# Performance work log

Hardware: AMD Instinct MI355X
Metric: run time of the kernel (lower is better)

Reference implementation:

```python
import jax, jax.numpy as jnp
import numpy as np

B = 256          # batch of molecules
N_ATOM = 1024    # atoms per molecule
N_EDGE = 8192    # directed edges per molecule (avg degree 8)
NEG_SLOPE = 0.01 # torch LeakyReLU default


def setup_inputs() -> dict:
    key = jax.random.key(0)
    ks = jax.random.split(key, 8)
    x = jax.random.normal(ks[0], (B, 3 * N_ATOM), dtype=jnp.float32)
    edge_index = jax.random.randint(ks[1], (2, N_EDGE), 0, N_ATOM, dtype=jnp.int64)
    # GCNConv weights (Glorot-ish small scale) and biases
    W1 = jax.random.normal(ks[2], (3, 64), dtype=jnp.float32) * 0.3
    b1 = jnp.zeros((64,), jnp.float32)
    W2 = jax.random.normal(ks[3], (64, 64), dtype=jnp.float32) * 0.1
    b2 = jnp.zeros((64,), jnp.float32)
    # project MLP: Linear(64,128) + LeakyReLU
    Wp = jax.random.normal(ks[4], (64, 128), dtype=jnp.float32) * 0.1
    bp = jnp.zeros((128,), jnp.float32)
    return {"x": x, "edge_index": edge_index, "W1": W1, "b1": b1,
            "W2": W2, "b2": b2, "Wp": Wp, "bp": bp}


def _leaky_relu(v):
    return jnp.where(v >= 0, v, NEG_SLOPE * v)


def reference(x, edge_index, W1, b1, W2, b2, Wp, bp):
    # x: [B, 3*n_atom] -> node features [B, n_atom, 3]
    bsz, n_feat = x.shape
    n = n_feat // 3
    h = x.reshape(bsz, n, 3)

    src = edge_index[0]  # message sources
    dst = edge_index[1]  # aggregation targets

    # GCN normalization with self-loops: deg[i] = 1 + in-degree(i)
    ones_e = jnp.ones((src.shape[0],), x.dtype)
    deg = jax.ops.segment_sum(ones_e, dst, num_segments=n) + 1.0
    dinv = jax.lax.rsqrt(deg)                # deg^{-1/2}, deg >= 1
    norm_e = dinv[src] * dinv[dst]           # [E]
    norm_self = dinv * dinv                  # self-loop weight per node

    def gcn(h, W, b):
        hw = h @ W                                        # [B, n, d_out]
        msg = hw[:, src, :] * norm_e[None, :, None]       # [B, E, d_out]
        agg = jax.vmap(lambda m: jax.ops.segment_sum(m, dst, num_segments=n))(msg)
        return agg + norm_self[None, :, None] * hw + b

    h = _leaky_relu(gcn(h, W1, b1))
    h = _leaky_relu(gcn(h, W2, b2))

    # global_mean_pool: every graph has exactly n atoms -> mean over atom axis
    g = h.mean(axis=1)                                    # [B, 64]

    # project MLP: Linear + LeakyReLU
    return _leaky_relu(g @ Wp + bp)                       # [B, 128]
```

## Files before the change

### kernel.cpp

```cpp
#include <hip/hip_runtime.h>

#define N_ATOMS 1024
#define N_EDGES 8192
#define EPAD    (N_EDGES + N_ATOMS)
#define NBATCH  256
#define NEG     0.01f

typedef unsigned int u32;
typedef __attribute__((ext_vector_type(2))) float f32x2;
typedef __attribute__((ext_vector_type(4))) float f32x4;
typedef __attribute__((ext_vector_type(8))) _Float16 f16x8;

__device__ __forceinline__ u32 pkrtz(float lo, float hi) {
    u32 r;
    asm("v_cvt_pkrtz_f16_f32 %0, %1, %2" : "=v"(r) : "v"(lo), "v"(hi));
    return r;
}
#define FMIX_LO(a, w, u) \
    asm("v_fma_mix_f32 %0, %1, %2, %0 op_sel_hi:[0,1,0]" : "+v"(a) : "v"(w), "v"(u))
#define FMIX_HI(a, w, u) \
    asm("v_fma_mix_f32 %0, %1, %2, %0 op_sel:[0,1,0] op_sel_hi:[0,1,0]" : "+v"(a) : "v"(w), "v"(u))

#define ROWPTR_OFF 0
#define COLW_OFF   4352
#define SELFW_OFF  (4352 + 73728)
#define PERM_OFF   (SELFW_OFF + 4096)
#define W2T_OFF    (PERM_OFF + 4096)

#define TSTR_B 144
#define SM_TILE_BYTES (N_ATOMS * TSTR_B)
#define SM_CT_OFF SM_TILE_BYTES
#define SM_TOTAL (SM_TILE_BYTES + 16384)

__global__ __launch_bounds__(1024) void build_csr(
    const int* __restrict__ ei,
    int*  __restrict__ rowptr,
    int2* __restrict__ colw,
    float* __restrict__ selfw_g,
    int*  __restrict__ perm_g,
    u32*  __restrict__ w2t,
    const float* __restrict__ W2)
{
    __shared__ int   sdeg[N_ATOMS];
    __shared__ int   sstart[N_ATOMS];
    __shared__ float sdinv[N_ATOMS];
    __shared__ int   wtot[16];
    __shared__ int   hist[128];
    const int t = threadIdx.x;
    const int lane = t & 63;
    const int w = t >> 6;
    const int* srcA = ei;
    const int* dstA = ei + N_EDGES;

    sdeg[t] = 0;
    if (t < 128) hist[t] = 0;
    for (int e = t; e < EPAD; e += 1024) colw[e] = make_int2(0, 0);
    __syncthreads();
    for (int e = t; e < N_EDGES; e += 1024) atomicAdd(&sdeg[dstA[e]], 1);
    __syncthreads();

    const int deg  = sdeg[t];
    const int pdeg = (deg + 1) & ~1;
    int v = pdeg;
    #pragma unroll
    for (int d = 1; d < 64; d <<= 1) {
        int u = __shfl_up(v, d, 64);
        if (lane >= d) v += u;
    }
    if (lane == 63) wtot[w] = v;
    __syncthreads();
    if (t == 0) {
        int run = 0;
        #pragma unroll
        for (int i = 0; i < 16; ++i) { int c = wtot[i]; wtot[i] = run; run += c; }
    }
    __syncthreads();
    const int start = v - pdeg + wtot[w];
    sstart[t] = start;
    const float dv = rsqrtf((float)deg + 1.0f);
    sdinv[t] = dv;
    rowptr[t] = start;
    if (t == N_ATOMS - 1) rowptr[N_ATOMS] = start + pdeg;
    selfw_g[t] = dv * dv;

    #pragma unroll
    for (int i = 0; i < 2; ++i) {
        const int idx = t + i * 1024;
        const int c = idx >> 5, kk = idx & 31;
        w2t[c * 32 + kk] = pkrtz(W2[(2 * kk) * 64 + c], W2[(2 * kk + 1) * 64 + c]);
    }

    const int dcl = deg < 127 ? deg : 127;
    atomicAdd(&hist[dcl], 1);
    sdeg[t] = 0;
    __syncthreads();
    if (t == 0) {
        int run = 0;
        for (int i = 0; i < 128; ++i) { int c = hist[i]; hist[i] = run; run += c; }
    }
    __syncthreads();
    const int pos = atomicAdd(&hist[dcl], 1);
    perm_g[pos] = t;
    __syncthreads();

    for (int e = t; e < N_EDGES; e += 1024) {
        const int d = dstA[e];
        const int s = srcA[e];
        const int slot = atomicAdd(&sdeg[d], 1);
        const float wgt = sdinv[s] * sdinv[d];
        colw[sstart[d] + slot] = make_int2(s, __float_as_int(wgt));
    }
}

__global__ __launch_bounds__(1024, 4) void gnn_main(
    const float* __restrict__ x,
    const int*  __restrict__ rowptr,
    const int2* __restrict__ colw,
    const float* __restrict__ selfw_g,
    const int*  __restrict__ perm_g,
    const float* __restrict__ W1, const float* __restrict__ b1,
    const u32*  __restrict__ w2t, const float* __restrict__ b2,
    const float* __restrict__ Wp, const float* __restrict__ bp,
    float* __restrict__ out)
{
    extern __shared__ char smem[];
    float4* ctile4 = (float4*)(smem + SM_CT_OFF);
    float*  paux   = (float*)ctile4;
    float*  wpool  = paux;
    float*  gvec   = paux + 1024;
    float*  proj   = paux + 1088;

    const int t = threadIdx.x;
    const int b = blockIdx.x;
    const float* xb = x + (size_t)b * (3 * N_ATOMS);

    const int atom = perm_g[t];
    const int s0 = rowptr[atom], s1 = rowptr[atom + 1];
    const float sw = selfw_g[atom];

    {
        float4 c;
        c.x = xb[3 * t]; c.y = xb[3 * t + 1]; c.z = xb[3 * t + 2]; c.w = 0.0f;
        ctile4[t] = c;
    }
    __syncthreads();

    u32 pw[32];
    {
        const float4 cs = ctile4[atom];
        float A0 = sw * cs.x, A1 = sw * cs.y, A2 = sw * cs.z;
        int4 cur = make_int4(0, 0, 0, 0);
        if (s0 < s1) cur = *(const int4*)(colw + s0);
        for (int j = s0; j < s1; j += 2) {
            const int jn = (j + 2 < s1) ? (j + 2) : s0;
            const int4 nxt = *(const int4*)(colw + jn);
            const float4 c0 = ctile4[cur.x];
            const float4 c1 = ctile4[cur.z];
            const float w0 = __int_as_float(cur.y), w1 = __int_as_float(cur.w);
            A0 += w0 * c0.x + w1 * c1.x;
            A1 += w0 * c0.y + w1 * c1.y;
            A2 += w0 * c0.z + w1 * c1.z;
            cur = nxt;
        }
        #pragma unroll
        for (int p = 0; p < 32; ++p) {
            f32x2 vv = *(const f32x2*)(b1 + 2 * p);
            vv = __builtin_elementwise_fma((f32x2){A0, A0}, *(const f32x2*)(W1 + 2 * p), vv);
            vv = __builtin_elementwise_fma((f32x2){A1, A1}, *(const f32x2*)(W1 + 64 + 2 * p), vv);
            vv = __builtin_elementwise_fma((f32x2){A2, A2}, *(const f32x2*)(W1 + 128 + 2 * p), vv);
            vv.x = fmaxf(vv.x, NEG * vv.x);
            vv.y = fmaxf(vv.y, NEG * vv.y);
            pw[p] = pkrtz(vv.x, vv.y);
        }
        uint4* trow = (uint4*)(smem + (size_t)atom * TSTR_B);
        #pragma unroll
        for (int q = 0; q < 8; ++q)
            trow[q] = make_uint4(pw[4 * q], pw[4 * q + 1], pw[4 * q + 2], pw[4 * q + 3]);
    }
    __syncthreads();

    float acc[64];
    {
        #pragma unroll
        for (int f = 0; f < 64; ++f) acc[f] = 0.0f;
        #pragma unroll
        for (int p = 0; p < 32; ++p) {
            FMIX_LO(acc[2 * p],     sw, pw[p]);
            FMIX_HI(acc[2 * p + 1], sw, pw[p]);
        }
        int4 cur = make_int4(0, 0, 0, 0);
        if (s0 < s1) cur = *(const int4*)(colw + s0);
        for (int j = s0; j < s1; j += 2) {
            const int jn = (j + 2 < s1) ? (j + 2) : s0;
            const int4 nxt = *(const int4*)(colw + jn);
            const uint4* rA = (const uint4*)(smem + (size_t)cur.x * TSTR_B);
            const uint4* rB = (const uint4*)(smem + (size_t)cur.z * TSTR_B);
            const float wA = __int_as_float(cur.y);
            const float wB = __int_as_float(cur.w);
            #pragma unroll
            for (int m = 0; m < 8; ++m) {
                const uint4 qA = rA[m];
                FMIX_LO(acc[8*m+0], wA, qA.x); FMIX_HI(acc[8*m+1], wA, qA.x);
                FMIX_LO(acc[8*m+2], wA, qA.y); FMIX_HI(acc[8*m+3], wA, qA.y);
                FMIX_LO(acc[8*m+4], wA, qA.z); FMIX_HI(acc[8*m+5], wA, qA.z);
                FMIX_LO(acc[8*m+6], wA, qA.w); FMIX_HI(acc[8*m+7], wA, qA.w);
            }
            #pragma unroll
            for (int m = 0; m < 8; ++m) {
                const uint4 qB = rB[m];
                FMIX_LO(acc[8*m+0], wB, qB.x); FMIX_HI(acc[8*m+1], wB, qB.x);
                FMIX_LO(acc[8*m+2], wB, qB.y); FMIX_HI(acc[8*m+3], wB, qB.y);
                FMIX_LO(acc[8*m+4], wB, qB.z); FMIX_HI(acc[8*m+5], wB, qB.z);
                FMIX_LO(acc[8*m+6], wB, qB.w); FMIX_HI(acc[8*m+7], wB, qB.w);
            }
            cur = nxt;
        }
    }
    __syncthreads();

    {
        u32 pb[32];
        #pragma unroll
        for (int p = 0; p < 32; ++p) pb[p] = pkrtz(acc[2 * p], acc[2 * p + 1]);
        uint4* trow = (uint4*)(smem + (size_t)atom * TSTR_B);
        #pragma unroll
        for (int q = 0; q < 8; ++q)
            trow[q] = make_uint4(pb[4 * q], pb[4 * q + 1], pb[4 * q + 2], pb[4 * q + 3]);
    }

    {
        const int l15 = t & 15;
        const int lq  = (t & 63) >> 4;
        const int w   = t >> 6;

        f16x8 wf[2][4];
        #pragma unroll
        for (int kt = 0; kt < 2; ++kt)
            #pragma unroll
            for (int ct = 0; ct < 4; ++ct)
                wf[kt][ct] = *(const f16x8*)(w2t + (ct * 16 + l15) * 32 + kt * 16 + lq * 4);
        float bias[4];
        #pragma unroll
        for (int ct = 0; ct < 4; ++ct) bias[ct] = b2[ct * 16 + l15];

        float pool[4] = {0.f, 0.f, 0.f, 0.f};
        #pragma unroll
        for (int rt = 0; rt < 4; ++rt) {
            const int arow = __shfl(atom, rt * 16 + l15, 64);
            const char* ab = smem + (size_t)arow * TSTR_B + lq * 16;
            const f16x8 a0 = *(const f16x8*)(ab);
            const f16x8 a1 = *(const f16x8*)(ab + 64);
            #pragma unroll
            for (int ct = 0; ct < 4; ++ct) {
                f32x4 cf = {0.f, 0.f, 0.f, 0.f};
                cf = __builtin_amdgcn_mfma_f32_16x16x32_f16(a0, wf[0][ct], cf, 0, 0, 0);
                cf = __builtin_amdgcn_mfma_f32_16x16x32_f16(a1, wf[1][ct], cf, 0, 0, 0);
                float s = 0.0f;
                #pragma unroll
                for (int r = 0; r < 4; ++r) {
                    const float vv = cf[r] + bias[ct];
                    s += fmaxf(vv, NEG * vv);
                }
                pool[ct] += s;
            }
        }
        #pragma unroll
        for (int ct = 0; ct < 4; ++ct) {
            pool[ct] += __shfl_xor(pool[ct], 16, 64);
            pool[ct] += __shfl_xor(pool[ct], 32, 64);
        }
        if ((t & 63) < 16) {
            #pragma unroll
            for (int ct = 0; ct < 4; ++ct)
                wpool[w * 64 + ct * 16 + l15] = pool[ct];
        }
    }
    __syncthreads();

    if (t < 64) {
        float s = 0.0f;
        #pragma unroll
        for (int w = 0; w < 16; ++w) s += wpool[w * 64 + t];
        gvec[t] = s * (1.0f / 1024.0f);
    }
    __syncthreads();
    if (t < 512) {
        const int col = t & 127, pc = t >> 7;
        float s = 0.0f;
        #pragma unroll
        for (int f = 0; f < 16; ++f)
            s += gvec[pc * 16 + f] * Wp[(pc * 16 + f) * 128 + col];
        proj[pc * 128 + col] = s;
    }
    __syncthreads();
    if (t < 128) {
        float s = bp[t] + proj[t] + proj[128 + t] + proj[256 + t] + proj[384 + t];
        s = fmaxf(s, NEG * s);
        out[(size_t)b * 128 + t] = s;
    }
}

extern "C" void kernel_launch(void* const* d_in, const int* in_sizes, int n_in,
                              void* d_out, int out_size, void* d_ws, size_t ws_size,
                              hipStream_t stream) {
    const float* x  = (const float*)d_in[0];
    const int*   ei = (const int*)  d_in[1];
    const float* W1 = (const float*)d_in[2];
    const float* b1 = (const float*)d_in[3];
    const float* W2 = (const float*)d_in[4];
    const float* b2 = (const float*)d_in[5];
    const float* Wp = (const float*)d_in[6];
    const float* bp = (const float*)d_in[7];
    float* out = (float*)d_out;

    char* ws = (char*)d_ws;
    int*   rowptr = (int*)  (ws + ROWPTR_OFF);
    int2*  colw   = (int2*) (ws + COLW_OFF);
    float* selfw  = (float*)(ws + SELFW_OFF);
    int*   perm   = (int*)  (ws + PERM_OFF);
    u32*   w2t    = (u32*)  (ws + W2T_OFF);

    build_csr<<<1, 1024, 0, stream>>>(ei, rowptr, colw, selfw, perm, w2t, W2);

    (void)hipFuncSetAttribute((const void*)gnn_main,
                              hipFuncAttributeMaxDynamicSharedMemorySize, SM_TOTAL);
    gnn_main<<<NBATCH, 1024, SM_TOTAL, stream>>>(
        x, rowptr, colw, selfw, perm, W1, b1, w2t, b2, Wp, bp, out);
}
```

Measured before the change: 39.28 us.

## Split second-layer aggregation across 8 lanes per atom by feature slice

The layer-2 neighbor aggregation is restructured so each atom is handled by 8 threads, each accumulating a 16-byte (8-feature) slice over 8 atoms, instead of one thread accumulating all 64 features for one atom. This cuts per-thread accumulator registers from 64 to 8 per atom, which should help occupancy. It also spreads LDS row reads across lanes and balances degree variation differently. The atom-to-row mapping for the MFMA stage now comes from a shared-memory table rather than a shuffle, at the cost of an extra store and more colw/rowptr global reads, since each edge list is now read by 8 lanes.

```diff
diff --git a/kernel.cpp b/kernel.cpp
--- a/kernel.cpp
+++ b/kernel.cpp
@@ -129,14 +129,11 @@
     float*  wpool  = paux;
     float*  gvec   = paux + 1024;
     float*  proj   = paux + 1088;
+    int*    satom  = (int*)(paux + 1600);
 
     const int t = threadIdx.x;
     const int b = blockIdx.x;
     const float* xb = x + (size_t)b * (3 * N_ATOMS);
-
-    const int atom = perm_g[t];
-    const int s0 = rowptr[atom], s1 = rowptr[atom + 1];
-    const float sw = selfw_g[atom];
 
     {
         float4 c;
@@ -145,8 +142,10 @@
     }
     __syncthreads();
 
-    u32 pw[32];
     {
+        const int atom = perm_g[t];
+        const int s0 = rowptr[atom], s1 = rowptr[atom + 1];
+        const float sw = selfw_g[atom];
         const float4 cs = ctile4[atom];
         float A0 = sw * cs.x, A1 = sw * cs.y, A2 = sw * cs.z;
         int4 cur = make_int4(0, 0, 0, 0);
@@ -162,6 +161,7 @@
             A2 += w0 * c0.z + w1 * c1.z;
             cur = nxt;
         }
+        u32 pw[32];
         #pragma unroll
         for (int p = 0; p < 32; ++p) {
             f32x2 vv = *(const f32x2*)(b1 + 2 * p);
@@ -179,59 +179,72 @@
     }
     __syncthreads();
 
-    float acc[64];
-    {
-        #pragma unroll
-        for (int f = 0; f < 64; ++f) acc[f] = 0.0f;
-        #pragma unroll
-        for (int p = 0; p < 32; ++p) {
-            FMIX_LO(acc[2 * p],     sw, pw[p]);
-            FMIX_HI(acc[2 * p + 1], sw, pw[p]);
-        }
-        int4 cur = make_int4(0, 0, 0, 0);
-        if (s0 < s1) cur = *(const int4*)(colw + s0);
-        for (int j = s0; j < s1; j += 2) {
-            const int jn = (j + 2 < s1) ? (j + 2) : s0;
-            const int4 nxt = *(const int4*)(colw + jn);
-            const uint4* rA = (const uint4*)(smem + (size_t)cur.x * TSTR_B);
-            const uint4* rB = (const uint4*)(smem + (size_t)cur.z * TSTR_B);
-            const float wA = __int_as_float(cur.y);
-            const float wB = __int_as_float(cur.w);
-            #pragma unroll
-            for (int m = 0; m < 8; ++m) {
-                const uint4 qA = rA[m];
-                FMIX_LO(acc[8*m+0], wA, qA.x); FMIX_HI(acc[8*m+1], wA, qA.x);
-                FMIX_LO(acc[8*m+2], wA, qA.y); FMIX_HI(acc[8*m+3], wA, qA.y);
-                FMIX_LO(acc[8*m+4], wA, qA.z); FMIX_HI(acc[8*m+5], wA, qA.z);
-                FMIX_LO(acc[8*m+6], wA, qA.w); FMIX_HI(acc[8*m+7], wA, qA.w);
-            }
-            #pragma unroll
-            for (int m = 0; m < 8; ++m) {
-                const uint4 qB = rB[m];
-                FMIX_LO(acc[8*m+0], wB, qB.x); FMIX_HI(acc[8*m+1], wB, qB.x);
-                FMIX_LO(acc[8*m+2], wB, qB.y); FMIX_HI(acc[8*m+3], wB, qB.y);
-                FMIX_LO(acc[8*m+4], wB, qB.z); FMIX_HI(acc[8*m+5], wB, qB.z);
-                FMIX_LO(acc[8*m+6], wB, qB.w); FMIX_HI(acc[8*m+7], wB, qB.w);
-            }
-            cur = nxt;
-        }
-    }
-    __syncthreads();
-
-    {
-        u32 pb[32];
-        #pragma unroll
-        for (int p = 0; p < 32; ++p) pb[p] = pkrtz(acc[2 * p], acc[2 * p + 1]);
-        uint4* trow = (uint4*)(smem + (size_t)atom * TSTR_B);
-        #pragma unroll
-        for (int q = 0; q < 8; ++q)
-            trow[q] = make_uint4(pb[4 * q], pb[4 * q + 1], pb[4 * q + 2], pb[4 * q + 3]);
-    }
+    const int w   = t >> 6;
+    const int g   = (t & 63) >> 3;
+    const int m   = t & 7;
+    const int mo  = m * 16;
+
+    int atoms[8];
+    #pragma unroll
+    for (int k = 0; k < 8; ++k) atoms[k] = perm_g[k * 128 + w * 8 + g];
+    int s0a[8], s1a[8];
+    #pragma unroll
+    for (int k = 0; k < 8; ++k) {
+        s0a[k] = rowptr[atoms[k]];
+        s1a[k] = rowptr[atoms[k] + 1];
+    }
+
+    u32 pr[8][4];
+    #pragma unroll
+    for (int k = 0; k < 8; ++k) {
+        const int atom = atoms[k];
+        float acc[8];
+        #pragma unroll
+        for (int f = 0; f < 8; ++f) acc[f] = 0.0f;
+        {
+            const float swk = selfw_g[atom];
+            const uint4 sv = *(const uint4*)(smem + (size_t)atom * TSTR_B + mo);
+            FMIX_LO(acc[0], swk, sv.x); FMIX_HI(acc[1], swk, sv.x);
+            FMIX_LO(acc[2], swk, sv.y); FMIX_HI(acc[3], swk, sv.y);
+            FMIX_LO(acc[4], swk, sv.z); FMIX_HI(acc[5], swk, sv.z);
+            FMIX_LO(acc[6], swk, sv.w); FMIX_HI(acc[7], swk, sv.w);
+        }
+        for (int j = s0a[k]; j < s1a[k]; j += 2) {
+            const int4 cw = *(const int4*)(colw + j);
+            const uint4 qA = *(const uint4*)(smem + (size_t)cw.x * TSTR_B + mo);
+            const uint4 qB = *(const uint4*)(smem + (size_t)cw.z * TSTR_B + mo);
+            const float wA = __int_as_float(cw.y);
+            const float wB = __int_as_float(cw.w);
+            FMIX_LO(acc[0], wA, qA.x); FMIX_HI(acc[1], wA, qA.x);
+            FMIX_LO(acc[2], wA, qA.y); FMIX_HI(acc[3], wA, qA.y);
+            FMIX_LO(acc[4], wA, qA.z); FMIX_HI(acc[5], wA, qA.z);
+            FMIX_LO(acc[6], wA, qA.w); FMIX_HI(acc[7], wA, qA.w);
+            FMIX_LO(acc[0], wB, qB.x); FMIX_HI(acc[1], wB, qB.x);
+            FMIX_LO(acc[2], wB, qB.y); FMIX_HI(acc[3], wB, qB.y);
+            FMIX_LO(acc[4], wB, qB.z); FMIX_HI(acc[5], wB, qB.z);
+            FMIX_LO(acc[6], wB, qB.w); FMIX_HI(acc[7], wB, qB.w);
+        }
+        pr[k][0] = pkrtz(acc[0], acc[1]);
+        pr[k][1] = pkrtz(acc[2], acc[3]);
+        pr[k][2] = pkrtz(acc[4], acc[5]);
+        pr[k][3] = pkrtz(acc[6], acc[7]);
+    }
+    __syncthreads();
+
+    #pragma unroll
+    for (int k = 0; k < 8; ++k) {
+        *(uint4*)(smem + (size_t)atoms[k] * TSTR_B + mo) =
+            make_uint4(pr[k][0], pr[k][1], pr[k][2], pr[k][3]);
+    }
+    if (m == 0) {
+        #pragma unroll
+        for (int k = 0; k < 8; ++k) satom[w * 64 + k * 8 + g] = atoms[k];
+    }
+    __syncthreads();
 
     {
         const int l15 = t & 15;
         const int lq  = (t & 63) >> 4;
-        const int w   = t >> 6;
 
         f16x8 wf[2][4];
         #pragma unroll
@@ -246,7 +259,7 @@
         float pool[4] = {0.f, 0.f, 0.f, 0.f};
         #pragma unroll
         for (int rt = 0; rt < 4; ++rt) {
-            const int arow = __shfl(atom, rt * 16 + l15, 64);
+            const int arow = satom[w * 64 + rt * 16 + l15];
             const char* ab = smem + (size_t)arow * TSTR_B + lq * 16;
             const f16x8 a0 = *(const f16x8*)(ab);
             const f16x8 a1 = *(const f16x8*)(ab + 64);
@@ -280,7 +293,7 @@
     if (t < 64) {
         float s = 0.0f;
         #pragma unroll
-        for (int w = 0; w < 16; ++w) s += wpool[w * 64 + t];
+        for (int ww = 0; ww < 16; ++ww) s += wpool[ww * 64 + t];
         gvec[t] = s * (1.0f / 1024.0f);
     }
     __syncthreads();
```

Result: slower. 41.93 us (+6.7%).

## Split fused GNN kernel into h1, gather and projection kernels via global fp16 buffer

Applied to the files above, without the earlier changes.

The single per-molecule kernel, which needed about 160 KB of LDS and ran one block per molecule, is split into three kernels. k_h1 writes layer-1 fp16 features to a 32 MB global workspace. k_gather runs 8 blocks per molecule, with the block index swizzled by XCD, and reads neighbour rows from global/L2. It applies the W2 MFMA and accumulates the pooled sums with atomics. k_proj then does the final projection. The aim is higher occupancy and parallelism than the LDS-bound single block gave, at the cost of extra global memory traffic, more kernel launches and float atomics that make results order-dependent.

```diff
diff --git a/kernel.cpp b/kernel.cpp
--- a/kernel.cpp
+++ b/kernel.cpp
@@ -26,11 +26,8 @@
 #define SELFW_OFF  (4352 + 73728)
 #define PERM_OFF   (SELFW_OFF + 4096)
 #define W2T_OFF    (PERM_OFF + 4096)
-
-#define TSTR_B 144
-#define SM_TILE_BYTES (N_ATOMS * TSTR_B)
-#define SM_CT_OFF SM_TILE_BYTES
-#define SM_TOTAL (SM_TILE_BYTES + 16384)
+#define H1_OFF     131072
+#define POOL_OFF   (H1_OFF + 33554432)
 
 __global__ __launch_bounds__(1024) void build_csr(
     const int* __restrict__ ei,
@@ -39,7 +36,8 @@
     float* __restrict__ selfw_g,
     int*  __restrict__ perm_g,
     u32*  __restrict__ w2t,
-    const float* __restrict__ W2)
+    const float* __restrict__ W2,
+    float* __restrict__ pool)
 {
     __shared__ int   sdeg[N_ATOMS];
     __shared__ int   sstart[N_ATOMS];
@@ -54,7 +52,8 @@
 
     sdeg[t] = 0;
     if (t < 128) hist[t] = 0;
-    for (int e = t; e < EPAD; e += 1024) colw[e] = make_int2(0, 0);
+    #pragma unroll
+    for (int i = t; i < NBATCH * 64; i += 1024) pool[i] = 0.0f;
     __syncthreads();
     for (int e = t; e < N_EDGES; e += 1024) atomicAdd(&sdeg[dstA[e]], 1);
     __syncthreads();
@@ -82,6 +81,7 @@
     rowptr[t] = start;
     if (t == N_ATOMS - 1) rowptr[N_ATOMS] = start + pdeg;
     selfw_g[t] = dv * dv;
+    if (deg & 1) colw[start + deg] = make_int2(0, 0);
 
     #pragma unroll
     for (int i = 0; i < 2; ++i) {
@@ -112,31 +112,19 @@
     }
 }
 
-__global__ __launch_bounds__(1024, 4) void gnn_main(
+__global__ __launch_bounds__(1024) void k_h1(
     const float* __restrict__ x,
     const int*  __restrict__ rowptr,
     const int2* __restrict__ colw,
     const float* __restrict__ selfw_g,
     const int*  __restrict__ perm_g,
     const float* __restrict__ W1, const float* __restrict__ b1,
-    const u32*  __restrict__ w2t, const float* __restrict__ b2,
-    const float* __restrict__ Wp, const float* __restrict__ bp,
-    float* __restrict__ out)
+    char* __restrict__ h1b)
 {
-    extern __shared__ char smem[];
-    float4* ctile4 = (float4*)(smem + SM_CT_OFF);
-    float*  paux   = (float*)ctile4;
-    float*  wpool  = paux;
-    float*  gvec   = paux + 1024;
-    float*  proj   = paux + 1088;
-
+    __shared__ float4 ctile4[N_ATOMS];
     const int t = threadIdx.x;
     const int b = blockIdx.x;
     const float* xb = x + (size_t)b * (3 * N_ATOMS);
-
-    const int atom = perm_g[t];
-    const int s0 = rowptr[atom], s1 = rowptr[atom + 1];
-    const float sw = selfw_g[atom];
 
     {
         float4 c;
@@ -145,93 +133,123 @@
     }
     __syncthreads();
 
+    const int atom = perm_g[t];
+    const int s0 = rowptr[atom], s1 = rowptr[atom + 1];
+    const float sw = selfw_g[atom];
+    const float4 cs = ctile4[atom];
+    float A0 = sw * cs.x, A1 = sw * cs.y, A2 = sw * cs.z;
+    int4 cur = make_int4(0, 0, 0, 0);
+    if (s0 < s1) cur = *(const int4*)(colw + s0);
+    for (int j = s0; j < s1; j += 2) {
+        const int jn = (j + 2 < s1) ? (j + 2) : s0;
+        const int4 nxt = *(const int4*)(colw + jn);
+        const float4 c0 = ctile4[cur.x];
+        const float4 c1 = ctile4[cur.z];
+        const float w0 = __int_as_float(cur.y), w1 = __int_as_float(cur.w);
+        A0 += w0 * c0.x + w1 * c1.x;
+        A1 += w0 * c0.y + w1 * c1.y;
+        A2 += w0 * c0.z + w1 * c1.z;
+        cur = nxt;
+    }
     u32 pw[32];
+    #pragma unroll
+    for (int p = 0; p < 32; ++p) {
+        f32x2 vv = *(const f32x2*)(b1 + 2 * p);
+        vv = __builtin_elementwise_fma((f32x2){A0, A0}, *(const f32x2*)(W1 + 2 * p), vv);
+        vv = __builtin_elementwise_fma((f32x2){A1, A1}, *(const f32x2*)(W1 + 64 + 2 * p), vv);
+        vv = __builtin_elementwise_fma((f32x2){A2, A2}, *(const f32x2*)(W1 + 128 + 2 * p), vv);
+        vv.x = fmaxf(vv.x, NEG * vv.x);
+        vv.y = fmaxf(vv.y, NEG * vv.y);
+        pw[p] = pkrtz(vv.x, vv.y);
+    }
+    uint4* row = (uint4*)(h1b + ((size_t)b << 17) + (size_t)atom * 128);
+    #pragma unroll
+    for (int q = 0; q < 8; ++q)
+        row[q] = make_uint4(pw[4 * q], pw[4 * q + 1], pw[4 * q + 2], pw[4 * q + 3]);
+}
+
+__global__ __launch_bounds__(256, 5) void k_gather(
+    const char* __restrict__ h1b,
+    const int*  __restrict__ rowptr,
+    const int2* __restrict__ colw,
+    const float* __restrict__ selfw_g,
+    const int*  __restrict__ perm_g,
+    const u32*  __restrict__ w2t, const float* __restrict__ b2,
+    float* __restrict__ pool)
+{
+    __shared__ char stg[128 * 144];
+    const int bid = blockIdx.x;
+    const int xcd = bid & 7, inner = bid >> 3;
+    const int seg = inner & 7, m32 = inner >> 3;
+    const int b = xcd + (m32 << 3);
+    const char* h1 = h1b + ((size_t)b << 17);
+
+    const int t = threadIdx.x;
+    const int slot = t >> 1, half = t & 1;
+    const int ho = half * 64;
+
+    const int atom = perm_g[slot * 8 + seg];
+    const int r0 = rowptr[atom];
+    const int np = (rowptr[atom + 1] - r0) >> 1;
+    const float swk = selfw_g[atom];
+
+    float acc[32];
+    #pragma unroll
+    for (int f = 0; f < 32; ++f) acc[f] = 0.0f;
+
     {
-        const float4 cs = ctile4[atom];
-        float A0 = sw * cs.x, A1 = sw * cs.y, A2 = sw * cs.z;
-        int4 cur = make_int4(0, 0, 0, 0);
-        if (s0 < s1) cur = *(const int4*)(colw + s0);
-        for (int j = s0; j < s1; j += 2) {
-            const int jn = (j + 2 < s1) ? (j + 2) : s0;
-            const int4 nxt = *(const int4*)(colw + jn);
-            const float4 c0 = ctile4[cur.x];
-            const float4 c1 = ctile4[cur.z];
-            const float w0 = __int_as_float(cur.y), w1 = __int_as_float(cur.w);
-            A0 += w0 * c0.x + w1 * c1.x;
-            A1 += w0 * c0.y + w1 * c1.y;
-            A2 += w0 * c0.z + w1 * c1.z;
-            cur = nxt;
-        }
-        #pragma unroll
-        for (int p = 0; p < 32; ++p) {
-            f32x2 vv = *(const f32x2*)(b1 + 2 * p);
-            vv = __builtin_elementwise_fma((f32x2){A0, A0}, *(const f32x2*)(W1 + 2 * p), vv);
-            vv = __builtin_elementwise_fma((f32x2){A1, A1}, *(const f32x2*)(W1 + 64 + 2 * p), vv);
-            vv = __builtin_elementwise_fma((f32x2){A2, A2}, *(const f32x2*)(W1 + 128 + 2 * p), vv);
-            vv.x = fmaxf(vv.x, NEG * vv.x);
-            vv.y = fmaxf(vv.y, NEG * vv.y);
-            pw[p] = pkrtz(vv.x, vv.y);
-        }
-        uint4* trow = (uint4*)(smem + (size_t)atom * TSTR_B);
-        #pragma unroll
-        for (int q = 0; q < 8; ++q)
-            trow[q] = make_uint4(pw[4 * q], pw[4 * q + 1], pw[4 * q + 2], pw[4 * q + 3]);
-    }
-    __syncthreads();
-
-    float acc[64];
+        const uint4* own = (const uint4*)(h1 + (size_t)atom * 128 + ho);
+        #pragma unroll
+        for (int q = 0; q < 4; ++q) {
+            const uint4 sv = own[q];
+            FMIX_LO(acc[q*8+0], swk, sv.x); FMIX_HI(acc[q*8+1], swk, sv.x);
+            FMIX_LO(acc[q*8+2], swk, sv.y); FMIX_HI(acc[q*8+3], swk, sv.y);
+            FMIX_LO(acc[q*8+4], swk, sv.z); FMIX_HI(acc[q*8+5], swk, sv.z);
+            FMIX_LO(acc[q*8+6], swk, sv.w); FMIX_HI(acc[q*8+7], swk, sv.w);
+        }
+    }
+    int4 cur = make_int4(0, 0, 0, 0);
+    if (np > 0) cur = *(const int4*)(colw + r0);
+    for (int j = 0; j < np; ++j) {
+        const int4 nxt = (j + 1 < np) ? *(const int4*)(colw + r0 + 2 * (j + 1)) : cur;
+        const uint4* rA = (const uint4*)(h1 + (size_t)cur.x * 128 + ho);
+        const uint4* rB = (const uint4*)(h1 + (size_t)cur.z * 128 + ho);
+        const float wA = __int_as_float(cur.y);
+        const float wB = __int_as_float(cur.w);
+        #pragma unroll
+        for (int q = 0; q < 4; ++q) {
+            const uint4 qa = rA[q];
+            FMIX_LO(acc[q*8+0], wA, qa.x); FMIX_HI(acc[q*8+1], wA, qa.x);
+            FMIX_LO(acc[q*8+2], wA, qa.y); FMIX_HI(acc[q*8+3], wA, qa.y);
+            FMIX_LO(acc[q*8+4], wA, qa.z); FMIX_HI(acc[q*8+5], wA, qa.z);
+            FMIX_LO(acc[q*8+6], wA, qa.w); FMIX_HI(acc[q*8+7], wA, qa.w);
+        }
+        #pragma unroll
+        for (int q = 0; q < 4; ++q) {
+            const uint4 qb = rB[q];
+            FMIX_LO(acc[q*8+0], wB, qb.x); FMIX_HI(acc[q*8+1], wB, qb.x);
+            FMIX_LO(acc[q*8+2], wB, qb.y); FMIX_HI(acc[q*8+3], wB, qb.y);
+            FMIX_LO(acc[q*8+4], wB, qb.z); FMIX_HI(acc[q*8+5], wB, qb.z);
+            FMIX_LO(acc[q*8+6], wB, qb.w); FMIX_HI(acc[q*8+7], wB, qb.w);
+        }
+        cur = nxt;
+    }
+
     {
-        #pragma unroll
-        for (int f = 0; f < 64; ++f) acc[f] = 0.0f;
-        #pragma unroll
-        for (int p = 0; p < 32; ++p) {
-            FMIX_LO(acc[2 * p],     sw, pw[p]);
-            FMIX_HI(acc[2 * p + 1], sw, pw[p]);
-        }
-        int4 cur = make_int4(0, 0, 0, 0);
-        if (s0 < s1) cur = *(const int4*)(colw + s0);
-        for (int j = s0; j < s1; j += 2) {
-            const int jn = (j + 2 < s1) ? (j + 2) : s0;
-            const int4 nxt = *(const int4*)(colw + jn);
-            const uint4* rA = (const uint4*)(smem + (size_t)cur.x * TSTR_B);
-            const uint4* rB = (const uint4*)(smem + (size_t)cur.z * TSTR_B);
-            const float wA = __int_as_float(cur.y);
-            const float wB = __int_as_float(cur.w);
-            #pragma unroll
-            for (int m = 0; m < 8; ++m) {
-                const uint4 qA = rA[m];
-                FMIX_LO(acc[8*m+0], wA, qA.x); FMIX_HI(acc[8*m+1], wA, qA.x);
-                FMIX_LO(acc[8*m+2], wA, qA.y); FMIX_HI(acc[8*m+3], wA, qA.y);
-                FMIX_LO(acc[8*m+4], wA, qA.z); FMIX_HI(acc[8*m+5], wA, qA.z);
-                FMIX_LO(acc[8*m+6], wA, qA.w); FMIX_HI(acc[8*m+7], wA, qA.w);
-            }
-            #pragma unroll
-            for (int m = 0; m < 8; ++m) {
-                const uint4 qB = rB[m];
-                FMIX_LO(acc[8*m+0], wB, qB.x); FMIX_HI(acc[8*m+1], wB, qB.x);
-                FMIX_LO(acc[8*m+2], wB, qB.y); FMIX_HI(acc[8*m+3], wB, qB.y);
-                FMIX_LO(acc[8*m+4], wB, qB.z); FMIX_HI(acc[8*m+5], wB, qB.z);
-                FMIX_LO(acc[8*m+6], wB, qB.w); FMIX_HI(acc[8*m+7], wB, qB.w);
-            }
-            cur = nxt;
-        }
+        u32 pk[16];
+        #pragma unroll
+        for (int i = 0; i < 16; ++i) pk[i] = pkrtz(acc[2 * i], acc[2 * i + 1]);
+        uint4* srow = (uint4*)(stg + slot * 144 + ho);
+        #pragma unroll
+        for (int q = 0; q < 4; ++q)
+            srow[q] = make_uint4(pk[4 * q], pk[4 * q + 1], pk[4 * q + 2], pk[4 * q + 3]);
     }
     __syncthreads();
 
     {
-        u32 pb[32];
-        #pragma unroll
-        for (int p = 0; p < 32; ++p) pb[p] = pkrtz(acc[2 * p], acc[2 * p + 1]);
-        uint4* trow = (uint4*)(smem + (size_t)atom * TSTR_B);
-        #pragma unroll
-        for (int q = 0; q < 8; ++q)
-            trow[q] = make_uint4(pb[4 * q], pb[4 * q + 1], pb[4 * q + 2], pb[4 * q + 3]);
-    }
-
-    {
+        const int w   = t >> 6;
         const int l15 = t & 15;
         const int lq  = (t & 63) >> 4;
-        const int w   = t >> 6;
 
         f16x8 wf[2][4];
         #pragma unroll
@@ -243,11 +261,11 @@
         #pragma unroll
         for (int ct = 0; ct < 4; ++ct) bias[ct] = b2[ct * 16 + l15];
 
-        float pool[4] = {0.f, 0.f, 0.f, 0.f};
-        #pragma unroll
-        for (int rt = 0; rt < 4; ++rt) {
-            const int arow = __shfl(atom, rt * 16 + l15, 64);
-            const char* ab = smem + (size_t)arow * TSTR_B + lq * 16;
+        float pool4[4] = {0.f, 0.f, 0.f, 0.f};
+        #pragma unroll
+        for (int rt = 0; rt < 2; ++rt) {
+            const int row = w * 32 + rt * 16 + l15;
+            const char* ab = stg + row * 144 + lq * 16;
             const f16x8 a0 = *(const f16x8*)(ab);
             const f16x8 a1 = *(const f16x8*)(ab + 64);
             #pragma unroll
@@ -261,43 +279,35 @@
                     const float vv = cf[r] + bias[ct];
                     s += fmaxf(vv, NEG * vv);
                 }
-                pool[ct] += s;
+                pool4[ct] += s;
             }
         }
         #pragma unroll
         for (int ct = 0; ct < 4; ++ct) {
-            pool[ct] += __shfl_xor(pool[ct], 16, 64);
-            pool[ct] += __shfl_xor(pool[ct], 32, 64);
+            pool4[ct] += __shfl_xor(pool4[ct], 16, 64);
+            pool4[ct] += __shfl_xor(pool4[ct], 32, 64);
         }
         if ((t & 63) < 16) {
             #pragma unroll
             for (int ct = 0; ct < 4; ++ct)
-                wpool[w * 64 + ct * 16 + l15] = pool[ct];
-        }
-    }
-    __syncthreads();
-
-    if (t < 64) {
-        float s = 0.0f;
-        #pragma unroll
-        for (int w = 0; w < 16; ++w) s += wpool[w * 64 + t];
-        gvec[t] = s * (1.0f / 1024.0f);
-    }
-    __syncthreads();
-    if (t < 512) {
-        const int col = t & 127, pc = t >> 7;
-        float s = 0.0f;
-        #pragma unroll
-        for (int f = 0; f < 16; ++f)
-            s += gvec[pc * 16 + f] * Wp[(pc * 16 + f) * 128 + col];
-        proj[pc * 128 + col] = s;
-    }
-    __syncthreads();
-    if (t < 128) {
-        float s = bp[t] + proj[t] + proj[128 + t] + proj[256 + t] + proj[384 + t];
-        s = fmaxf(s, NEG * s);
-        out[(size_t)b * 128 + t] = s;
-    }
+                atomicAdd(&pool[b * 64 + ct * 16 + l15], pool4[ct]);
+        }
+    }
+}
+
+__global__ __launch_bounds__(128) void k_proj(
+    const float* __restrict__ pool,
+    const float* __restrict__ Wp, const float* __restrict__ bp,
+    float* __restrict__ out)
+{
+    const int b = blockIdx.x;
+    const int t = threadIdx.x;
+    float s = bp[t];
+    #pragma unroll
+    for (int f = 0; f < 64; ++f)
+        s += (pool[b * 64 + f] * (1.0f / 1024.0f)) * Wp[f * 128 + t];
+    s = fmaxf(s, NEG * s);
+    out[(size_t)b * 128 + t] = s;
 }
 
 extern "C" void kernel_launch(void* const* d_in, const int* in_sizes, int n_in,
@@ -319,11 +329,11 @@
     float* selfw  = (float*)(ws + SELFW_OFF);
     int*   perm   = (int*)  (ws + PERM_OFF);
     u32*   w2t    = (u32*)  (ws + W2T_OFF);
-
-    build_csr<<<1, 1024, 0, stream>>>(ei, rowptr, colw, selfw, perm, w2t, W2);
-
-    (void)hipFuncSetAttribute((const void*)gnn_main,
-                              hipFuncAttributeMaxDynamicSharedMemorySize, SM_TOTAL);
-    gnn_main<<<NBATCH, 1024, SM_TOTAL, stream>>>(
-        x, rowptr, colw, selfw, perm, W1, b1, w2t, b2, Wp, bp, out);
-}
+    char*  h1b    = ws + H1_OFF;
+    float* pool   = (float*)(ws + POOL_OFF);
+
+    build_csr<<<1, 1024, 0, stream>>>(ei, rowptr, colw, selfw, perm, w2t, W2, pool);
+    k_h1<<<NBATCH, 1024, 0, stream>>>(x, rowptr, colw, selfw, perm, W1, b1, h1b);
+    k_gather<<<NBATCH * 8, 256, 0, stream>>>(h1b, rowptr, colw, selfw, perm, w2t, b2, pool);
+    k_proj<<<NBATCH, 128, 0, stream>>>(pool, Wp, bp, out);
+}
```

Result: slower. 95.08 us (+142.1%).

## Split layer-2 aggregation across thread pairs with half-width feature rows

Applied to the files above, without the earlier changes.

Each thread now aggregates 32 of the 64 features for two atoms (thread pairs share one atom) instead of all 64 for one atom, which halves the accumulator registers and software-pipelines the LDS row loads ahead of the fma_mix work. The layer-1 coordinate tile is stored as float2 plus float instead of float4, shrinking shared memory. The full padding clear of colw in build_csr is replaced by writing only the one padding slot per odd-degree atom. The cost is doing the edge-index loads twice, and the MFMA row mapping must be remapped to the new atom assignment.

```diff
diff --git a/kernel.cpp b/kernel.cpp
--- a/kernel.cpp
+++ b/kernel.cpp
@@ -2,7 +2,6 @@
 
 #define N_ATOMS 1024
 #define N_EDGES 8192
-#define EPAD    (N_EDGES + N_ATOMS)
 #define NBATCH  256
 #define NEG     0.01f
 
@@ -29,8 +28,8 @@
 
 #define TSTR_B 144
 #define SM_TILE_BYTES (N_ATOMS * TSTR_B)
-#define SM_CT_OFF SM_TILE_BYTES
-#define SM_TOTAL (SM_TILE_BYTES + 16384)
+#define SM_AUX_OFF SM_TILE_BYTES
+#define SM_TOTAL (SM_TILE_BYTES + 12288)
 
 __global__ __launch_bounds__(1024) void build_csr(
     const int* __restrict__ ei,
@@ -54,7 +53,6 @@
 
     sdeg[t] = 0;
     if (t < 128) hist[t] = 0;
-    for (int e = t; e < EPAD; e += 1024) colw[e] = make_int2(0, 0);
     __syncthreads();
     for (int e = t; e < N_EDGES; e += 1024) atomicAdd(&sdeg[dstA[e]], 1);
     __syncthreads();
@@ -82,6 +80,7 @@
     rowptr[t] = start;
     if (t == N_ATOMS - 1) rowptr[N_ATOMS] = start + pdeg;
     selfw_g[t] = dv * dv;
+    if (deg & 1) colw[start + deg] = make_int2(0, 0);
 
     #pragma unroll
     for (int i = 0; i < 2; ++i) {
@@ -111,6 +110,32 @@
         colw[sstart[d] + slot] = make_int2(s, __float_as_int(wgt));
     }
 }
+
+#define FMIX_SET(q0, q1, q2, q3, wt)                                  \
+    do {                                                              \
+        FMIX_LO(acc[0],  wt, (q0).x); FMIX_HI(acc[1],  wt, (q0).x);   \
+        FMIX_LO(acc[2],  wt, (q0).y); FMIX_HI(acc[3],  wt, (q0).y);   \
+        FMIX_LO(acc[4],  wt, (q0).z); FMIX_HI(acc[5],  wt, (q0).z);   \
+        FMIX_LO(acc[6],  wt, (q0).w); FMIX_HI(acc[7],  wt, (q0).w);   \
+        FMIX_LO(acc[8],  wt, (q1).x); FMIX_HI(acc[9],  wt, (q1).x);   \
+        FMIX_LO(acc[10], wt, (q1).y); FMIX_HI(acc[11], wt, (q1).y);   \
+        FMIX_LO(acc[12], wt, (q1).z); FMIX_HI(acc[13], wt, (q1).z);   \
+        FMIX_LO(acc[14], wt, (q1).w); FMIX_HI(acc[15], wt, (q1).w);   \
+        FMIX_LO(acc[16], wt, (q2).x); FMIX_HI(acc[17], wt, (q2).x);   \
+        FMIX_LO(acc[18], wt, (q2).y); FMIX_HI(acc[19], wt, (q2).y);   \
+        FMIX_LO(acc[20], wt, (q2).z); FMIX_HI(acc[21], wt, (q2).z);   \
+        FMIX_LO(acc[22], wt, (q2).w); FMIX_HI(acc[23], wt, (q2).w);   \
+        FMIX_LO(acc[24], wt, (q3).x); FMIX_HI(acc[25], wt, (q3).x);   \
+        FMIX_LO(acc[26], wt, (q3).y); FMIX_HI(acc[27], wt, (q3).y);   \
+        FMIX_LO(acc[28], wt, (q3).z); FMIX_HI(acc[29], wt, (q3).z);   \
+        FMIX_LO(acc[30], wt, (q3).w); FMIX_HI(acc[31], wt, (q3).w);   \
+    } while (0)
+
+#define LOAD_SET(q0, q1, q2, q3, rowbase)                 \
+    do {                                                  \
+        const uint4* _r = (const uint4*)(rowbase);        \
+        q0 = _r[0]; q1 = _r[1]; q2 = _r[2]; q3 = _r[3];   \
+    } while (0)
 
 __global__ __launch_bounds__(1024, 4) void gnn_main(
     const float* __restrict__ x,
@@ -124,44 +149,44 @@
     float* __restrict__ out)
 {
     extern __shared__ char smem[];
-    float4* ctile4 = (float4*)(smem + SM_CT_OFF);
-    float*  paux   = (float*)ctile4;
-    float*  wpool  = paux;
-    float*  gvec   = paux + 1024;
-    float*  proj   = paux + 1088;
+    float2* cx2 = (float2*)(smem + SM_AUX_OFF);
+    float*  cz  = (float*)(smem + SM_AUX_OFF + 8192);
+    float*  paux  = (float*)(smem + SM_AUX_OFF);
+    float*  wpool = paux;
+    float*  gvec  = paux + 1024;
+    float*  proj  = paux + 1088;
 
     const int t = threadIdx.x;
     const int b = blockIdx.x;
     const float* xb = x + (size_t)b * (3 * N_ATOMS);
 
-    const int atom = perm_g[t];
-    const int s0 = rowptr[atom], s1 = rowptr[atom + 1];
-    const float sw = selfw_g[atom];
-
     {
-        float4 c;
-        c.x = xb[3 * t]; c.y = xb[3 * t + 1]; c.z = xb[3 * t + 2]; c.w = 0.0f;
-        ctile4[t] = c;
-    }
-    __syncthreads();
-
-    u32 pw[32];
+        cx2[t] = make_float2(xb[3 * t], xb[3 * t + 1]);
+        cz[t]  = xb[3 * t + 2];
+    }
+    __syncthreads();
+
     {
-        const float4 cs = ctile4[atom];
-        float A0 = sw * cs.x, A1 = sw * cs.y, A2 = sw * cs.z;
+        const int atom = perm_g[t];
+        const int s0 = rowptr[atom], s1 = rowptr[atom + 1];
+        const float sw = selfw_g[atom];
+        const float2 cs = cx2[atom];
+        float A0 = sw * cs.x, A1 = sw * cs.y, A2 = sw * cz[atom];
         int4 cur = make_int4(0, 0, 0, 0);
         if (s0 < s1) cur = *(const int4*)(colw + s0);
         for (int j = s0; j < s1; j += 2) {
             const int jn = (j + 2 < s1) ? (j + 2) : s0;
             const int4 nxt = *(const int4*)(colw + jn);
-            const float4 c0 = ctile4[cur.x];
-            const float4 c1 = ctile4[cur.z];
+            const float2 c0 = cx2[cur.x];
+            const float2 c1 = cx2[cur.z];
+            const float z0 = cz[cur.x], z1 = cz[cur.z];
             const float w0 = __int_as_float(cur.y), w1 = __int_as_float(cur.w);
             A0 += w0 * c0.x + w1 * c1.x;
             A1 += w0 * c0.y + w1 * c1.y;
-            A2 += w0 * c0.z + w1 * c1.z;
+            A2 += w0 * z0 + w1 * z1;
             cur = nxt;
         }
+        u32 pw[32];
         #pragma unroll
         for (int p = 0; p < 32; ++p) {
             f32x2 vv = *(const f32x2*)(b1 + 2 * p);
@@ -179,74 +204,80 @@
     }
     __syncthreads();
 
-    float acc[64];
+    const int ho   = (t & 1) * 64;
+    const int pidx = t >> 1;
+
+    int atomR[2];
+    u32 pr[2][16];
+    const int2* colw2 = (const int2*)colw;
+
+    #pragma unroll
+    for (int r = 0; r < 2; ++r) {
+        const int atom = perm_g[r * 512 + pidx];
+        atomR[r] = atom;
+        const int s0e = rowptr[atom];
+        const int ne  = rowptr[atom + 1] - s0e;
+        const float swk = selfw_g[atom];
+
+        float acc[32];
+        #pragma unroll
+        for (int f = 0; f < 32; ++f) acc[f] = 0.0f;
+        {
+            uint4 s0q, s1q, s2q, s3q;
+            LOAD_SET(s0q, s1q, s2q, s3q, smem + (size_t)atom * TSTR_B + ho);
+            FMIX_SET(s0q, s1q, s2q, s3q, swk);
+        }
+        if (ne > 0) {
+            int2 cwA = colw2[s0e];
+            uint4 a0, a1, a2, a3, b0, b1_, b2_, b3;
+            LOAD_SET(a0, a1, a2, a3, smem + (size_t)cwA.x * TSTR_B + ho);
+            for (int j = 0; j < ne; j += 2) {
+                const int2 cwB = colw2[s0e + j + 1];
+                LOAD_SET(b0, b1_, b2_, b3, smem + (size_t)cwB.x * TSTR_B + ho);
+                FMIX_SET(a0, a1, a2, a3, __int_as_float(cwA.y));
+                if (j + 2 < ne) {
+                    cwA = colw2[s0e + j + 2];
+                    LOAD_SET(a0, a1, a2, a3, smem + (size_t)cwA.x * TSTR_B + ho);
+                }
+                FMIX_SET(b0, b1_, b2_, b3, __int_as_float(cwB.y));
+            }
+        }
+        #pragma unroll
+        for (int i = 0; i < 16; ++i) pr[r][i] = pkrtz(acc[2 * i], acc[2 * i + 1]);
+    }
+
+    const int l15 = t & 15;
+    const int lq  = (t & 63) >> 4;
+    const int w   = t >> 6;
+    f16x8 wf[2][4];
+    #pragma unroll
+    for (int kt = 0; kt < 2; ++kt)
+        #pragma unroll
+        for (int ct = 0; ct < 4; ++ct)
+            wf[kt][ct] = *(const f16x8*)(w2t + (ct * 16 + l15) * 32 + kt * 16 + lq * 4);
+    float bias[4];
+    #pragma unroll
+    for (int ct = 0; ct < 4; ++ct) bias[ct] = b2[ct * 16 + l15];
+
+    __syncthreads();
+
+    #pragma unroll
+    for (int r = 0; r < 2; ++r) {
+        uint4* dst = (uint4*)(smem + (size_t)atomR[r] * TSTR_B + ho);
+        dst[0] = make_uint4(pr[r][0],  pr[r][1],  pr[r][2],  pr[r][3]);
+        dst[1] = make_uint4(pr[r][4],  pr[r][5],  pr[r][6],  pr[r][7]);
+        dst[2] = make_uint4(pr[r][8],  pr[r][9],  pr[r][10], pr[r][11]);
+        dst[3] = make_uint4(pr[r][12], pr[r][13], pr[r][14], pr[r][15]);
+    }
+    __syncthreads();
+
     {
-        #pragma unroll
-        for (int f = 0; f < 64; ++f) acc[f] = 0.0f;
-        #pragma unroll
-        for (int p = 0; p < 32; ++p) {
-            FMIX_LO(acc[2 * p],     sw, pw[p]);
-            FMIX_HI(acc[2 * p + 1], sw, pw[p]);
-        }
-        int4 cur = make_int4(0, 0, 0, 0);
-        if (s0 < s1) cur = *(const int4*)(colw + s0);
-        for (int j = s0; j < s1; j += 2) {
-            const int jn = (j + 2 < s1) ? (j + 2) : s0;
-            const int4 nxt = *(const int4*)(colw + jn);
-            const uint4* rA = (const uint4*)(smem + (size_t)cur.x * TSTR_B);
-            const uint4* rB = (const uint4*)(smem + (size_t)cur.z * TSTR_B);
-            const float wA = __int_as_float(cur.y);
-            const float wB = __int_as_float(cur.w);
-            #pragma unroll
-            for (int m = 0; m < 8; ++m) {
-                const uint4 qA = rA[m];
-                FMIX_LO(acc[8*m+0], wA, qA.x); FMIX_HI(acc[8*m+1], wA, qA.x);
-                FMIX_LO(acc[8*m+2], wA, qA.y); FMIX_HI(acc[8*m+3], wA, qA.y);
-                FMIX_LO(acc[8*m+4], wA, qA.z); FMIX_HI(acc[8*m+5], wA, qA.z);
-                FMIX_LO(acc[8*m+6], wA, qA.w); FMIX_HI(acc[8*m+7], wA, qA.w);
-            }
-            #pragma unroll
-            for (int m = 0; m < 8; ++m) {
-                const uint4 qB = rB[m];
-                FMIX_LO(acc[8*m+0], wB, qB.x); FMIX_HI(acc[8*m+1], wB, qB.x);
-                FMIX_LO(acc[8*m+2], wB, qB.y); FMIX_HI(acc[8*m+3], wB, qB.y);
-                FMIX_LO(acc[8*m+4], wB, qB.z); FMIX_HI(acc[8*m+5], wB, qB.z);
-                FMIX_LO(acc[8*m+6], wB, qB.w); FMIX_HI(acc[8*m+7], wB, qB.w);
-            }
-            cur = nxt;
-        }
-    }
-    __syncthreads();
-
-    {
-        u32 pb[32];
-        #pragma unroll
-        for (int p = 0; p < 32; ++p) pb[p] = pkrtz(acc[2 * p], acc[2 * p + 1]);
-        uint4* trow = (uint4*)(smem + (size_t)atom * TSTR_B);
-        #pragma unroll
-        for (int q = 0; q < 8; ++q)
-            trow[q] = make_uint4(pb[4 * q], pb[4 * q + 1], pb[4 * q + 2], pb[4 * q + 3]);
-    }
-
-    {
-        const int l15 = t & 15;
-        const int lq  = (t & 63) >> 4;
-        const int w   = t >> 6;
-
-        f16x8 wf[2][4];
-        #pragma unroll
-        for (int kt = 0; kt < 2; ++kt)
-            #pragma unroll
-            for (int ct = 0; ct < 4; ++ct)
-                wf[kt][ct] = *(const f16x8*)(w2t + (ct * 16 + l15) * 32 + kt * 16 + lq * 4);
-        float bias[4];
-        #pragma unroll
-        for (int ct = 0; ct < 4; ++ct) bias[ct] = b2[ct * 16 + l15];
-
         float pool[4] = {0.f, 0.f, 0.f, 0.f};
         #pragma unroll
         for (int rt = 0; rt < 4; ++rt) {
-            const int arow = __shfl(atom, rt * 16 + l15, 64);
+            const int po = (rt & 1) ? (16 + l15) : l15;
+            const int arow = (rt < 2) ? __shfl(atomR[0], 2 * po, 64)
+                                      : __shfl(atomR[1], 2 * po, 64);
             const char* ab = smem + (size_t)arow * TSTR_B + lq * 16;
             const f16x8 a0 = *(const f16x8*)(ab);
             const f16x8 a1 = *(const f16x8*)(ab + 64);
@@ -257,8 +288,8 @@
                 cf = __builtin_amdgcn_mfma_f32_16x16x32_f16(a1, wf[1][ct], cf, 0, 0, 0);
                 float s = 0.0f;
                 #pragma unroll
-                for (int r = 0; r < 4; ++r) {
-                    const float vv = cf[r] + bias[ct];
+                for (int rr = 0; rr < 4; ++rr) {
+                    const float vv = cf[rr] + bias[ct];
                     s += fmaxf(vv, NEG * vv);
                 }
                 pool[ct] += s;
@@ -280,7 +311,7 @@
     if (t < 64) {
         float s = 0.0f;
         #pragma unroll
-        for (int w = 0; w < 16; ++w) s += wpool[w * 64 + t];
+        for (int ww = 0; ww < 16; ++ww) s += wpool[ww * 64 + t];
         gvec[t] = s * (1.0f / 1024.0f);
     }
     __syncthreads();
```

Measured after the change: 38.75 us. Within noise of the previous version (-1.4%).
